# Performance work log

Hardware: AMD Instinct MI355X
Metric: run time of the kernel (lower is better)

Reference implementation:

```python
import jax, jax.numpy as jnp
import numpy as np

EPS = 1e-5

def conv2d(x, w, b=None, pad=1):
    y = jax.lax.conv_general_dilated(x, w, (1, 1), ((pad, pad), (pad, pad)),
                                     dimension_numbers=('NCHW', 'OIHW', 'NCHW'))
    if b is not None:
        y = y + b[None, :, None, None]
    return y

def batchnorm(x, g, b):
    # torch training-mode BN: per-channel batch mean / biased variance
    m = x.mean((0, 2, 3), keepdims=True)
    v = ((x - m) ** 2).mean((0, 2, 3), keepdims=True)
    return (x - m) * jax.lax.rsqrt(v + EPS) * g[None, :, None, None] + b[None, :, None, None]

def deform_conv(x, offset, w):
    # x: [B,C,H,W]; offset: [B,2*K*K,H,W] as (dy,dx) pairs per kernel tap; w: [O,C,K,K]
    B, C, H, W = x.shape
    O = w.shape[0]
    K = w.shape[-1]
    off = offset.reshape(B, K * K, 2, H, W)
    ki = jnp.arange(K)
    ky, kx = jnp.meshgrid(ki, ki, indexing='ij')
    ky = ky.reshape(-1).astype(x.dtype)  # [K*K]
    kx = kx.reshape(-1).astype(x.dtype)
    gy = jnp.arange(H, dtype=x.dtype)[None, None, :, None]
    gx = jnp.arange(W, dtype=x.dtype)[None, None, None, :]
    pad = (K - 1) // 2  # stride=1, pad=1, dilation=1
    py = gy + (ky - pad)[None, :, None, None] + off[:, :, 0]  # [B,K*K,H,W]
    px = gx + (kx - pad)[None, :, None, None] + off[:, :, 1]
    y0 = jnp.floor(py)
    x0 = jnp.floor(px)
    wy = py - y0
    wx = px - x0
    y0i = y0.astype(jnp.int32)
    x0i = x0.astype(jnp.int32)
    xf = x.reshape(B, C, H * W)

    def corner(yc, xc):
        valid = ((yc >= 0) & (yc < H) & (xc >= 0) & (xc < W)).astype(x.dtype)
        idx = jnp.clip(yc, 0, H - 1) * W + jnp.clip(xc, 0, W - 1)  # [B,K*K,H,W]
        g = jax.vmap(lambda im, ix: im[:, ix])(xf, idx)  # [B,C,K*K,H,W]
        return g * valid[:, None]

    v00 = corner(y0i, x0i)
    v01 = corner(y0i, x0i + 1)
    v10 = corner(y0i + 1, x0i)
    v11 = corner(y0i + 1, x0i + 1)
    wy_ = wy[:, None]
    wx_ = wx[:, None]
    samp = (v00 * (1 - wy_) * (1 - wx_) + v01 * (1 - wy_) * wx_
            + v10 * wy_ * (1 - wx_) + v11 * wy_ * wx_)  # [B,C,K*K,H,W]
    return jnp.einsum('bckhw,ock->bohw', samp, w.reshape(O, C, K * K))


def setup_inputs() -> dict:
    key = jax.random.key(0)
    ks = jax.random.split(key, 20)
    B, inC, H, W = 64, 3, 64, 64
    G = 1  # num_deformable_groups

    def u(k, shape, fan):
        s = 1.0 / np.sqrt(fan)
        return jax.random.uniform(k, shape, jnp.float32, -s, s)

    return {
        'x':   jax.random.normal(ks[0], (B, inC, H, W), jnp.float32),
        'w1':  u(ks[1], (8, inC, 3, 3), inC * 9),
        'g1':  jnp.ones((8,), jnp.float32),  'b1': jnp.zeros((8,), jnp.float32),
        'w2':  u(ks[2], (20, 8, 3, 3), 8 * 9), 'bc2': u(ks[3], (20,), 8 * 9),
        'g2':  jnp.ones((20,), jnp.float32), 'b2': jnp.zeros((20,), jnp.float32),
        'w3':  u(ks[4], (G * 18, 20, 3, 3), 20 * 9),
        'wd1': u(ks[5], (40, 20, 3, 3), 20 * 9),
        'g3':  jnp.ones((40,), jnp.float32), 'b3': jnp.zeros((40,), jnp.float32),
        'w4':  u(ks[6], (G * 18, 40, 3, 3), 40 * 9), 'bc4': u(ks[7], (G * 18,), 40 * 9),
        'wd2': u(ks[8], (64, 40, 3, 3), 40 * 9),
        'g4':  jnp.ones((64,), jnp.float32), 'b4': jnp.zeros((64,), jnp.float32),
        'fw':  u(ks[9], (10, 256), 256), 'fb': u(ks[10], (10,), 256),
    }


def reference(x, w1, g1, b1, w2, bc2, g2, b2, w3, wd1, g3, b3, w4, bc4, wd2, g4, b4, fw, fb):
    h = batchnorm(jax.nn.relu(conv2d(x, w1)), g1, b1)
    h = batchnorm(jax.nn.relu(conv2d(h, w2, bc2)), g2, b2)
    off1 = conv2d(h, w3)
    h = batchnorm(jax.nn.relu(deform_conv(h, off1, wd1)), g3, b3)
    off2 = conv2d(h, w4, bc4)
    h = batchnorm(jax.nn.relu(deform_conv(h, off2, wd2)), g4, b4)
    em = h
    B, C, H, W = h.shape
    # avg_pool2d kernel [H//2, W//2] (stride defaults to kernel) -> 2x2 output
    p = h.reshape(B, C, 2, H // 2, 2, W // 2).mean(axis=(3, 5))  # [B,C,2,2]
    logits = p.reshape(B, -1) @ fw.T + fb  # [B,10]
    return jax.nn.softmax(logits, axis=-1), em
```

## Files before the change

kernel.cpp:

```cpp
#include <hip/hip_runtime.h>

#define IMW 64
#define HW 4096
#define BATCH 64
#define NPIX (BATCH * HW)
#define TPB 512
#define PIXBLK 8

__device__ inline float bfbits(unsigned int hi16) {
    union { unsigned int i; float f; } v; v.i = hi16; return v.f;
}
__device__ inline float bf_lo(unsigned int u) { return bfbits(u << 16); }
__device__ inline float bf_hi(unsigned int u) { return bfbits(u & 0xffff0000u); }
__device__ inline unsigned short f2bf(float f) {
    union { float f; unsigned int i; } v; v.f = f;
    unsigned int i = v.i;
    i += 0x7fff + ((i >> 16) & 1);
    return (unsigned short)(i >> 16);
}

__device__ inline unsigned pack_h2(float a, float b) {
    union { unsigned u; _Float16 h[2]; } v;
    v.h[0] = (_Float16)a;
    v.h[1] = (_Float16)b;
    return v.u;
}
__device__ inline float h_lo(unsigned u) {
    union { unsigned u; _Float16 h[2]; } v; v.u = u; return (float)v.h[0];
}
__device__ inline float h_hi(unsigned u) {
    union { unsigned u; _Float16 h[2]; } v; v.u = u; return (float)v.h[1];
}

template <int CO_BLOCKS>
__device__ inline void swz(int lin, int& img, int& xblk, int& cob) {
    const int per_img = PIXBLK * CO_BLOCKS;
    int xcd = lin & 7;
    int s = lin >> 3;
    img = xcd * 8 + s / per_img;
    int r = s % per_img;
    cob = r / PIXBLK;
    xblk = r % PIXBLK;
}

template <int CIN, int COUT, bool RELU, bool BIAS, bool AFF, bool IN_NCHW,
          bool IN_BF16, int OUT_MODE>
__global__ void conv3x3_k(const void* __restrict__ in_,
                          const float* __restrict__ w,
                          const float* __restrict__ bias,
                          const float* __restrict__ iscale,
                          const float* __restrict__ ishift,
                          void* __restrict__ out_) {
    __shared__ float lw[9 * CIN * COUT];
    __shared__ float lb[COUT];
    __shared__ float lsc[CIN];
    __shared__ float lsh[CIN];

    for (int dst = threadIdx.x; dst < 9 * CIN * COUT; dst += blockDim.x) {
        int co = dst % COUT;
        int kci = dst / COUT;
        int k = kci / CIN;
        int ci = kci % CIN;
        lw[dst] = w[(size_t)co * (CIN * 9) + ci * 9 + k];
    }
    if (threadIdx.x < COUT) lb[threadIdx.x] = BIAS ? bias[threadIdx.x] : 0.f;
    if (AFF && threadIdx.x < CIN) {
        lsc[threadIdx.x] = iscale[threadIdx.x];
        lsh[threadIdx.x] = ishift[threadIdx.x];
    }
    __syncthreads();

    int img, xblk, cob;
    swz<1>(blockIdx.x, img, xblk, cob);
    int b = img;
    int pos = xblk * TPB + threadIdx.x;
    int p = (b << 12) + pos;
    int y = pos >> 6;
    int x = pos & 63;

    float acc[COUT];
#pragma unroll
    for (int co = 0; co < COUT; ++co) acc[co] = lb[co];

#pragma unroll 1
    for (int k = 0; k < 9; ++k) {
        int ky = k / 3, kx = k - ky * 3;
        int yy = y + ky - 1, xx = x + kx - 1;
        if (yy < 0 || yy >= IMW || xx < 0 || xx >= IMW) continue;

        float vin[CIN];
        if constexpr (IN_NCHW) {
            const float* ip = (const float*)in_;
#pragma unroll
            for (int ci = 0; ci < CIN; ++ci)
                vin[ci] = ip[((size_t)(b * CIN + ci) << 12) + yy * IMW + xx];
        } else if constexpr (!IN_BF16) {
            const float* ip = (const float*)in_ + ((size_t)((b << 12) + yy * IMW + xx)) * CIN;
#pragma unroll
            for (int c4 = 0; c4 < CIN / 4; ++c4) {
                float4 v = *(const float4*)(ip + c4 * 4);
                vin[c4 * 4 + 0] = v.x;
                vin[c4 * 4 + 1] = v.y;
                vin[c4 * 4 + 2] = v.z;
                vin[c4 * 4 + 3] = v.w;
            }
        } else if constexpr (CIN % 8 == 0) {
            const uint4* ip = (const uint4*)((const unsigned short*)in_ +
                                             ((size_t)((b << 12) + yy * IMW + xx)) * CIN);
#pragma unroll
            for (int c8 = 0; c8 < CIN / 8; ++c8) {
                uint4 u = ip[c8];
                vin[c8 * 8 + 0] = bf_lo(u.x); vin[c8 * 8 + 1] = bf_hi(u.x);
                vin[c8 * 8 + 2] = bf_lo(u.y); vin[c8 * 8 + 3] = bf_hi(u.y);
                vin[c8 * 8 + 4] = bf_lo(u.z); vin[c8 * 8 + 5] = bf_hi(u.z);
                vin[c8 * 8 + 6] = bf_lo(u.w); vin[c8 * 8 + 7] = bf_hi(u.w);
            }
        } else {
            const uint2* ip = (const uint2*)((const unsigned short*)in_ +
                                             ((size_t)((b << 12) + yy * IMW + xx)) * CIN);
#pragma unroll
            for (int c4 = 0; c4 < CIN / 4; ++c4) {
                uint2 u = ip[c4];
                vin[c4 * 4 + 0] = bf_lo(u.x); vin[c4 * 4 + 1] = bf_hi(u.x);
                vin[c4 * 4 + 2] = bf_lo(u.y); vin[c4 * 4 + 3] = bf_hi(u.y);
            }
        }
        if constexpr (AFF) {
#pragma unroll
            for (int ci = 0; ci < CIN; ++ci)
                vin[ci] = fmaf(vin[ci], lsc[ci], lsh[ci]);
        }
#pragma unroll
        for (int ci = 0; ci < CIN; ++ci) {
            float s = vin[ci];
            const float* wr = &lw[(k * CIN + ci) * COUT];
#pragma unroll
            for (int co = 0; co < COUT; ++co)
                acc[co] = fmaf(wr[co], s, acc[co]);
        }
    }

    if (RELU) {
#pragma unroll
        for (int co = 0; co < COUT; ++co) acc[co] = fmaxf(acc[co], 0.f);
    }

    if constexpr (OUT_MODE == 2) {
        unsigned* o = (unsigned*)out_;
#pragma unroll
        for (int i = 0; i < COUT / 2; ++i)
            o[(size_t)i * NPIX + p] = pack_h2(acc[2 * i], acc[2 * i + 1]);
    } else if constexpr (OUT_MODE == 1) {
        unsigned int us[COUT / 2];
#pragma unroll
        for (int i = 0; i < COUT / 2; ++i)
            us[i] = (unsigned int)f2bf(acc[2 * i]) | ((unsigned int)f2bf(acc[2 * i + 1]) << 16);
        uint2* o2 = (uint2*)((unsigned short*)out_ + (size_t)p * COUT);
#pragma unroll
        for (int i = 0; i < COUT / 4; ++i)
            o2[i] = make_uint2(us[2 * i], us[2 * i + 1]);
    } else {
        float* op = (float*)out_ + (size_t)p * COUT;
        if constexpr (COUT % 4 == 0) {
#pragma unroll
            for (int c4 = 0; c4 < COUT / 4; ++c4)
                *(float4*)(op + c4 * 4) =
                    make_float4(acc[c4 * 4], acc[c4 * 4 + 1], acc[c4 * 4 + 2], acc[c4 * 4 + 3]);
        } else {
#pragma unroll
            for (int c2 = 0; c2 < COUT / 2; ++c2)
                *(float2*)(op + c2 * 2) = make_float2(acc[c2 * 2], acc[c2 * 2 + 1]);
        }
    }
}

template <int CIN, int COUT_TOT, int COUT_BLK, int CO_BLOCKS, bool OUT_NCHW, bool PERTAP>
__global__ void deform_k(const void* __restrict__ in_,
                         const unsigned* __restrict__ off,
                         const float* __restrict__ w,
                         const float* __restrict__ iscale,
                         const float* __restrict__ ishift,
                         void* __restrict__ out_) {
    constexpr int WSLICE = CIN * COUT_BLK;
    constexpr int LWSZ = PERTAP ? 2 * WSLICE : 9 * WSLICE;
    __shared__ float lw[LWSZ];
    __shared__ float lsc[CIN];
    __shared__ float lsh[CIN];

    int img, xblk, cob;
    swz<CO_BLOCKS>(blockIdx.x, img, xblk, cob);
    int co_base = cob * COUT_BLK;

    if (threadIdx.x < CIN) {
        lsc[threadIdx.x] = iscale[threadIdx.x];
        lsh[threadIdx.x] = ishift[threadIdx.x];
    }

    const float* wsrc = nullptr;
    if constexpr (PERTAP) {
        wsrc = w + (size_t)(co_base + (threadIdx.x & (COUT_BLK - 1))) * (CIN * 9) +
               (threadIdx.x / COUT_BLK) * 9;
    } else {
        for (int dst = threadIdx.x; dst < 9 * WSLICE; dst += blockDim.x) {
            int co = dst % COUT_BLK;
            int kci = dst / COUT_BLK;
            int k = kci / CIN;
            int ci = kci % CIN;
            lw[dst] = w[(size_t)(co_base + co) * (CIN * 9) + ci * 9 + k];
        }
    }

    constexpr int NFULL = WSLICE / TPB;
    constexpr int REM = WSLICE - NFULL * TPB;
    constexpr int CISTEP = TPB / COUT_BLK;

    auto stage_tap = [&](int k, int buf) {
        if constexpr (PERTAP) {
            const float* src = wsrc + k;
            float* d = lw + buf * WSLICE + threadIdx.x;
#pragma unroll
            for (int j = 0; j < NFULL; ++j)
                d[j * TPB] = src[(size_t)j * CISTEP * 9];
            if (REM > 0 && threadIdx.x < REM)
                d[NFULL * TPB] = src[(size_t)NFULL * CISTEP * 9];
        }
    };

    if constexpr (PERTAP) stage_tap(0, 0);
    __syncthreads();

    int b = img;
    int pos = xblk * TPB + threadIdx.x;
    int p = (b << 12) + pos;
    int y = pos >> 6;
    int x = pos & 63;

    float acc[COUT_BLK];
#pragma unroll
    for (int co = 0; co < COUT_BLK; ++co) acc[co] = 0.f;

    unsigned od[9];
#pragma unroll
    for (int j = 0; j < 9; ++j) od[j] = off[(size_t)j * NPIX + p];

    const unsigned short* ib = (const unsigned short*)in_ + (size_t)b * HW * CIN;

#pragma unroll 1
    for (int k = 0; k < 9; ++k) {
        if constexpr (PERTAP) {
            if (k < 8) stage_tap(k + 1, (k + 1) & 1);
        }
        const int kbase = PERTAP ? (k & 1) * CIN : k * CIN;

        int ky = k / 3, kx = k - ky * 3;
        float py = (float)(y + ky - 1) + h_lo(od[k]);
        float px = (float)(x + kx - 1) + h_hi(od[k]);
        float fy = floorf(py), fx = floorf(px);
        float wy = py - fy, wx = px - fx;
        int y0 = (int)fy, x0 = (int)fx;
        int y1 = y0 + 1, x1 = x0 + 1;
        bool vy0 = (unsigned)y0 < (unsigned)IMW;
        bool vy1 = (unsigned)y1 < (unsigned)IMW;
        bool vx0 = (unsigned)x0 < (unsigned)IMW;
        bool vx1 = (unsigned)x1 < (unsigned)IMW;
        int cy0 = min(max(y0, 0), IMW - 1), cy1 = min(max(y1, 0), IMW - 1);
        int cx0 = min(max(x0, 0), IMW - 1), cx1 = min(max(x1, 0), IMW - 1);
        float w00 = (1.f - wy) * (1.f - wx) * ((vy0 & vx0) ? 1.f : 0.f);
        float w01 = (1.f - wy) * wx * ((vy0 & vx1) ? 1.f : 0.f);
        float w10 = wy * (1.f - wx) * ((vy1 & vx0) ? 1.f : 0.f);
        float w11 = wy * wx * ((vy1 & vx1) ? 1.f : 0.f);
        float wsum = w00 + w01 + w10 + w11;

        if constexpr (CIN % 8 == 0) {
            const uint4* q00 = (const uint4*)(ib + (size_t)(cy0 * IMW + cx0) * CIN);
            const uint4* q01 = (const uint4*)(ib + (size_t)(cy0 * IMW + cx1) * CIN);
            const uint4* q10 = (const uint4*)(ib + (size_t)(cy1 * IMW + cx0) * CIN);
            const uint4* q11 = (const uint4*)(ib + (size_t)(cy1 * IMW + cx1) * CIN);
#pragma unroll 1
            for (int c8 = 0; c8 < CIN / 8; ++c8) {
                uint4 a = q00[c8], bq = q01[c8], c = q10[c8], d = q11[c8];
#pragma unroll
                for (int h = 0; h < 4; ++h) {
                    unsigned int ua = (&a.x)[h], ub = (&bq.x)[h];
                    unsigned int uc = (&c.x)[h], ud = (&d.x)[h];
                    int ci0 = c8 * 8 + h * 2;
                    float r0 = w00 * bf_lo(ua) + w01 * bf_lo(ub) +
                               w10 * bf_lo(uc) + w11 * bf_lo(ud);
                    float r1 = w00 * bf_hi(ua) + w01 * bf_hi(ub) +
                               w10 * bf_hi(uc) + w11 * bf_hi(ud);
                    float s0 = fmaf(r0, lsc[ci0], lsh[ci0] * wsum);
                    float s1 = fmaf(r1, lsc[ci0 + 1], lsh[ci0 + 1] * wsum);
                    const float* wr0 = &lw[(kbase + ci0) * COUT_BLK];
                    const float* wr1 = &lw[(kbase + ci0 + 1) * COUT_BLK];
#pragma unroll
                    for (int co = 0; co < COUT_BLK; ++co)
                        acc[co] = fmaf(wr0[co], s0, acc[co]);
#pragma unroll
                    for (int co = 0; co < COUT_BLK; ++co)
                        acc[co] = fmaf(wr1[co], s1, acc[co]);
                }
            }
        } else {
            const uint2* q00 = (const uint2*)(ib + (size_t)(cy0 * IMW + cx0) * CIN);
            const uint2* q01 = (const uint2*)(ib + (size_t)(cy0 * IMW + cx1) * CIN);
            const uint2* q10 = (const uint2*)(ib + (size_t)(cy1 * IMW + cx0) * CIN);
            const uint2* q11 = (const uint2*)(ib + (size_t)(cy1 * IMW + cx1) * CIN);
#pragma unroll
            for (int c4 = 0; c4 < CIN / 4; ++c4) {
                uint2 a = q00[c4], bq = q01[c4], c = q10[c4], d = q11[c4];
#pragma unroll
                for (int h = 0; h < 2; ++h) {
                    unsigned int ua = (&a.x)[h], ub = (&bq.x)[h];
                    unsigned int uc = (&c.x)[h], ud = (&d.x)[h];
                    int ci0 = c4 * 4 + h * 2;
                    float r0 = w00 * bf_lo(ua) + w01 * bf_lo(ub) +
                               w10 * bf_lo(uc) + w11 * bf_lo(ud);
                    float r1 = w00 * bf_hi(ua) + w01 * bf_hi(ub) +
                               w10 * bf_hi(uc) + w11 * bf_hi(ud);
                    float s0 = fmaf(r0, lsc[ci0], lsh[ci0] * wsum);
                    float s1 = fmaf(r1, lsc[ci0 + 1], lsh[ci0 + 1] * wsum);
                    const float* wr0 = &lw[(kbase + ci0) * COUT_BLK];
                    const float* wr1 = &lw[(kbase + ci0 + 1) * COUT_BLK];
#pragma unroll
                    for (int co = 0; co < COUT_BLK; ++co)
                        acc[co] = fmaf(wr0[co], s0, acc[co]);
#pragma unroll
                    for (int co = 0; co < COUT_BLK; ++co)
                        acc[co] = fmaf(wr1[co], s1, acc[co]);
                }
            }
        }

        if constexpr (PERTAP) __syncthreads();
    }

#pragma unroll
    for (int co = 0; co < COUT_BLK; ++co) acc[co] = fmaxf(acc[co], 0.f);

    if constexpr (OUT_NCHW) {
        float* o = (float*)out_;
#pragma unroll
        for (int co = 0; co < COUT_BLK; ++co)
            __builtin_nontemporal_store(acc[co],
                &o[((size_t)(b * COUT_TOT + co_base + co) << 12) + pos]);
    } else {
        unsigned int us[COUT_BLK / 2];
#pragma unroll
        for (int i = 0; i < COUT_BLK / 2; ++i)
            us[i] = (unsigned int)f2bf(acc[2 * i]) | ((unsigned int)f2bf(acc[2 * i + 1]) << 16);
        unsigned short* ob = (unsigned short*)out_ + (size_t)p * COUT_TOT + co_base;
        if constexpr (COUT_BLK % 8 == 0) {
            uint4* o4 = (uint4*)ob;
#pragma unroll
            for (int i = 0; i < COUT_BLK / 8; ++i)
                o4[i] = make_uint4(us[4 * i], us[4 * i + 1], us[4 * i + 2], us[4 * i + 3]);
        } else {
            uint2* o2 = (uint2*)ob;
#pragma unroll
            for (int i = 0; i < COUT_BLK / 4; ++i)
                o2[i] = make_uint2(us[2 * i], us[2 * i + 1]);
        }
    }
}

template <int C>
__global__ void bn_partial_nhwc(const float* __restrict__ src, float* __restrict__ sums) {
    const size_t total = (size_t)NPIX * C;
    size_t stride = (size_t)gridDim.x * blockDim.x;
    float s = 0.f, q = 0.f;
    for (size_t i = (size_t)blockIdx.x * blockDim.x + threadIdx.x; i < total; i += stride) {
        float v = src[i];
        s += v;
        q += v * v;
    }
    __shared__ float ls[320], lq[320];
    ls[threadIdx.x] = s;
    lq[threadIdx.x] = q;
    __syncthreads();
    if (threadIdx.x < C) {
        float a = 0.f, bb = 0.f;
        for (int j = threadIdx.x; j < 320; j += C) {
            a += ls[j];
            bb += lq[j];
        }
        atomicAdd(&sums[threadIdx.x], a);
        atomicAdd(&sums[C + threadIdx.x], bb);
    }
}

template <int C>
__global__ void bn_partial_nhwc_bf16(const unsigned short* __restrict__ src,
                                     float* __restrict__ sums) {
    const int CP = C / 2;
    const size_t totalu = (size_t)NPIX * CP;
    const unsigned int* s32 = (const unsigned int*)src;
    size_t stride = (size_t)gridDim.x * blockDim.x;
    float s0 = 0.f, q0 = 0.f, s1 = 0.f, q1 = 0.f;
    for (size_t i = (size_t)blockIdx.x * blockDim.x + threadIdx.x; i < totalu; i += stride) {
        unsigned int u = s32[i];
        float a = bf_lo(u), b = bf_hi(u);
        s0 += a; q0 += a * a;
        s1 += b; q1 += b * b;
    }
    __shared__ float l0[320], m0[320], l1[320], m1[320];
    l0[threadIdx.x] = s0; m0[threadIdx.x] = q0;
    l1[threadIdx.x] = s1; m1[threadIdx.x] = q1;
    __syncthreads();
    if (threadIdx.x < C) {
        int cp = threadIdx.x >> 1, hi = threadIdx.x & 1;
        float a = 0.f, bb = 0.f;
        for (int j = cp; j < 320; j += CP) {
            a += hi ? l1[j] : l0[j];
            bb += hi ? m1[j] : m0[j];
        }
        atomicAdd(&sums[threadIdx.x], a);
        atomicAdd(&sums[C + threadIdx.x], bb);
    }
}

__global__ void bn_partial_nchw(const float* __restrict__ src, int C, int parts,
                                float* __restrict__ sums) {
    int c = blockIdx.x / parts;
    int part = blockIdx.x % parts;
    int chunk = NPIX / parts;
    int start = part * chunk;
    float s = 0.f, q = 0.f;
    for (int i4 = start / 4 + threadIdx.x; i4 < (start + chunk) / 4; i4 += blockDim.x) {
        int p4 = i4 * 4;
        int bb = p4 >> 12, pos = p4 & 4095;
        float4 v = *(const float4*)&src[((size_t)(bb * C + c) << 12) + pos];
        s += v.x + v.y + v.z + v.w;
        q += v.x * v.x + v.y * v.y + v.z * v.z + v.w * v.w;
    }
    __shared__ float ls[256], lq[256];
    ls[threadIdx.x] = s;
    lq[threadIdx.x] = q;
    __syncthreads();
    for (int st = 128; st > 0; st >>= 1) {
        if (threadIdx.x < st) {
            ls[threadIdx.x] += ls[threadIdx.x + st];
            lq[threadIdx.x] += lq[threadIdx.x + st];
        }
        __syncthreads();
    }
    if (threadIdx.x == 0) {
        atomicAdd(&sums[c], ls[0]);
        atomicAdd(&sums[C + c], lq[0]);
    }
}

__global__ void bn_finalize_kernel(const float* __restrict__ sums, int C,
                                   const float* __restrict__ g,
                                   const float* __restrict__ b,
                                   float* __restrict__ scale,
                                   float* __restrict__ shift) {
    int c = threadIdx.x;
    if (c >= C) return;
    const float invN = 1.f / (float)NPIX;
    float mean = sums[c] * invN;
    float var = sums[C + c] * invN - mean * mean;
    float sc = g[c] * rsqrtf(var + 1e-5f);
    scale[c] = sc;
    shift[c] = b[c] - mean * sc;
}

__global__ void bn4_apply_pool(float* __restrict__ em,
                               const float* __restrict__ scale,
                               const float* __restrict__ shift,
                               float* __restrict__ pw) {
    int bc = blockIdx.x;
    int c = bc & 63;
    int t = threadIdx.x;
    float sc = scale[c], sh = shift[c];
    float* base = em + ((size_t)bc << 12);
    int pos = t * 16;
    int quad = ((pos >= 2048) ? 2 : 0) + ((pos & 63) >> 5);
    float s = 0.f;
#pragma unroll
    for (int k4 = 0; k4 < 4; ++k4) {
        float4 v = *(float4*)(base + pos + k4 * 4);
        v.x = fmaf(v.x, sc, sh);
        v.y = fmaf(v.y, sc, sh);
        v.z = fmaf(v.z, sc, sh);
        v.w = fmaf(v.w, sc, sh);
        *(float4*)(base + pos + k4 * 4) = v;
        s += v.x + v.y + v.z + v.w;
    }
    __shared__ float qs[4];
    if (t < 4) qs[t] = 0.f;
    __syncthreads();
    atomicAdd(&qs[quad], s);
    __syncthreads();
    if (t < 4) pw[bc * 4 + t] = qs[t] * (1.f / 1024.f);
}

__global__ void fc_softmax_kernel(const float* __restrict__ pw,
                                  const float* __restrict__ fw,
                                  const float* __restrict__ fb,
                                  float* __restrict__ out) {
    int b = blockIdx.x;
    int t = threadIdx.x;
    __shared__ float logits[10];
    if (t < 10) {
        float acc = fb[t];
        const float* p = pw + b * 256;
        for (int q = 0; q < 256; ++q) acc = fmaf(p[q], fw[t * 256 + q], acc);
        logits[t] = acc;
    }
    __syncthreads();
    if (t == 0) {
        float m = -1e30f;
        for (int q = 0; q < 10; ++q) m = fmaxf(m, logits[q]);
        float e[10], sum = 0.f;
        for (int q = 0; q < 10; ++q) { e[q] = expf(logits[q] - m); sum += e[q]; }
        float inv = 1.f / sum;
        for (int q = 0; q < 10; ++q) out[b * 10 + q] = e[q] * inv;
    }
}

extern "C" void kernel_launch(void* const* d_in, const int* in_sizes, int n_in,
                              void* d_out, int out_size, void* d_ws, size_t ws_size,
                              hipStream_t stream) {
    (void)in_sizes; (void)n_in; (void)out_size; (void)ws_size;

    const float* x   = (const float*)d_in[0];
    const float* w1  = (const float*)d_in[1];
    const float* g1  = (const float*)d_in[2];
    const float* b1  = (const float*)d_in[3];
    const float* w2  = (const float*)d_in[4];
    const float* bc2 = (const float*)d_in[5];
    const float* g2  = (const float*)d_in[6];
    const float* b2  = (const float*)d_in[7];
    const float* w3  = (const float*)d_in[8];
    const float* wd1 = (const float*)d_in[9];
    const float* g3  = (const float*)d_in[10];
    const float* b3  = (const float*)d_in[11];
    const float* w4  = (const float*)d_in[12];
    const float* bc4 = (const float*)d_in[13];
    const float* wd2 = (const float*)d_in[14];
    const float* g4  = (const float*)d_in[15];
    const float* b4  = (const float*)d_in[16];
    const float* fw  = (const float*)d_in[17];
    const float* fb  = (const float*)d_in[18];

    float* out = (float*)d_out;
    float* softout = out;
    float* em = out + 640;

    float* ws = (float*)d_ws;
    float* h1 = ws;
    unsigned short* h2b = (unsigned short*)(h1 + (size_t)2097152);
    unsigned short* h3b = h2b + (size_t)5242880;
    unsigned* offu = (unsigned*)(h3b + (size_t)10485760);
    float* sums1 = (float*)(offu + (size_t)9 * NPIX);
    float* sums2 = sums1 + 128;
    float* sums3 = sums2 + 128;
    float* sums4 = sums3 + 128;
    float* scale = sums4 + 128;
    float* shift = scale + 64;
    float* pw = shift + 64;

    dim3 blk(TPB);
    dim3 gpix(BATCH * PIXBLK);

    hipMemsetAsync(sums1, 0, 4 * 128 * sizeof(float), stream);

    conv3x3_k<3, 8, true, false, false, true, false, 0>
        <<<gpix, blk, 0, stream>>>(x, w1, nullptr, nullptr, nullptr, h1);
    bn_partial_nhwc<8><<<256, 320, 0, stream>>>(h1, sums1);
    bn_finalize_kernel<<<1, 64, 0, stream>>>(sums1, 8, g1, b1, scale, shift);

    conv3x3_k<8, 20, true, true, true, false, false, 1>
        <<<gpix, blk, 0, stream>>>(h1, w2, bc2, scale, shift, h2b);
    bn_partial_nhwc_bf16<20><<<256, 320, 0, stream>>>(h2b, sums2);
    bn_finalize_kernel<<<1, 64, 0, stream>>>(sums2, 20, g2, b2, scale, shift);

    conv3x3_k<20, 18, false, false, true, false, true, 2>
        <<<gpix, blk, 0, stream>>>(h2b, w3, nullptr, scale, shift, offu);
    deform_k<20, 40, 20, 2, false, false>
        <<<dim3(BATCH * PIXBLK * 2), blk, 0, stream>>>(h2b, offu, wd1, scale, shift, h3b);
    bn_partial_nhwc_bf16<40><<<256, 320, 0, stream>>>(h3b, sums3);
    bn_finalize_kernel<<<1, 64, 0, stream>>>(sums3, 40, g3, b3, scale, shift);

    conv3x3_k<40, 18, false, true, true, false, true, 2>
        <<<gpix, blk, 0, stream>>>(h3b, w4, bc4, scale, shift, offu);
    deform_k<40, 64, 32, 2, true, true>
        <<<dim3(BATCH * PIXBLK * 2), blk, 0, stream>>>(h3b, offu, wd2, scale, shift, em);
    bn_partial_nchw<<<64 * 32, 256, 0, stream>>>(em, 64, 32, sums4);
    bn_finalize_kernel<<<1, 64, 0, stream>>>(sums4, 64, g4, b4, scale, shift);

    bn4_apply_pool<<<64 * 64, 256, 0, stream>>>(em, scale, shift, pw);
    fc_softmax_kernel<<<64, 64, 0, stream>>>(pw, fw, fb, softout);
}
```

Before: 594.2 us.

## Fuse BN statistics into conv/deform epilogues and stage final output in fp16

Removes the separate BN partial-sum kernels. Each conv and deform kernel now computes per-channel sum and sum-of-squares with wave shuffles and shared-memory atomics, then adds them into global sums with atomics. The last deform conv writes an fp16 raw buffer, which the apply/pool kernel reads and expands to fp32 em. This avoids re-reading the large intermediates but adds fp16 rounding to the final activations and many global atomics.

```diff
diff --git a/kernel.cpp b/kernel.cpp
--- a/kernel.cpp
+++ b/kernel.cpp
@@ -30,6 +30,9 @@
 }
 __device__ inline float h_hi(unsigned u) {
     union { unsigned u; _Float16 h[2]; } v; v.u = u; return (float)v.h[1];
+}
+__device__ inline unsigned short f2h(float f) {
+    union { _Float16 h; unsigned short u; } v; v.h = (_Float16)f; return v.u;
 }
 
 template <int CO_BLOCKS>
@@ -44,17 +47,19 @@
 }
 
 template <int CIN, int COUT, bool RELU, bool BIAS, bool AFF, bool IN_NCHW,
-          bool IN_BF16, int OUT_MODE>
+          bool IN_BF16, int OUT_MODE, bool FUSE_BN>
 __global__ void conv3x3_k(const void* __restrict__ in_,
                           const float* __restrict__ w,
                           const float* __restrict__ bias,
                           const float* __restrict__ iscale,
                           const float* __restrict__ ishift,
-                          void* __restrict__ out_) {
+                          void* __restrict__ out_,
+                          float* __restrict__ bnsums) {
     __shared__ float lw[9 * CIN * COUT];
     __shared__ float lb[COUT];
     __shared__ float lsc[CIN];
     __shared__ float lsh[CIN];
+    __shared__ float bnacc[FUSE_BN ? 2 * COUT : 1];
 
     for (int dst = threadIdx.x; dst < 9 * CIN * COUT; dst += blockDim.x) {
         int co = dst % COUT;
@@ -68,6 +73,7 @@
         lsc[threadIdx.x] = iscale[threadIdx.x];
         lsh[threadIdx.x] = ishift[threadIdx.x];
     }
+    if (FUSE_BN && threadIdx.x < 2 * COUT) bnacc[threadIdx.x] = 0.f;
     __syncthreads();
 
     int img, xblk, cob;
@@ -145,6 +151,23 @@
         for (int co = 0; co < COUT; ++co) acc[co] = fmaxf(acc[co], 0.f);
     }
 
+    if constexpr (FUSE_BN) {
+#pragma unroll
+        for (int co = 0; co < COUT; ++co) {
+            float s = acc[co];
+            float q = s * s;
+#pragma unroll
+            for (int off = 32; off; off >>= 1) {
+                s += __shfl_down(s, off, 64);
+                q += __shfl_down(q, off, 64);
+            }
+            if ((threadIdx.x & 63) == 0) {
+                atomicAdd(&bnacc[co], s);
+                atomicAdd(&bnacc[COUT + co], q);
+            }
+        }
+    }
+
     if constexpr (OUT_MODE == 2) {
         unsigned* o = (unsigned*)out_;
 #pragma unroll
@@ -172,20 +195,31 @@
                 *(float2*)(op + c2 * 2) = make_float2(acc[c2 * 2], acc[c2 * 2 + 1]);
         }
     }
-}
-
-template <int CIN, int COUT_TOT, int COUT_BLK, int CO_BLOCKS, bool OUT_NCHW, bool PERTAP>
+
+    if constexpr (FUSE_BN) {
+        __syncthreads();
+        if (threadIdx.x < COUT)
+            atomicAdd(&bnsums[threadIdx.x], bnacc[threadIdx.x]);
+        else if (threadIdx.x < 2 * COUT)
+            atomicAdd(&bnsums[threadIdx.x], bnacc[threadIdx.x]);
+    }
+}
+
+template <int CIN, int COUT_TOT, int COUT_BLK, int CO_BLOCKS, bool OUT_NCHW,
+          bool PERTAP, bool FUSE>
 __global__ void deform_k(const void* __restrict__ in_,
                          const unsigned* __restrict__ off,
                          const float* __restrict__ w,
                          const float* __restrict__ iscale,
                          const float* __restrict__ ishift,
-                         void* __restrict__ out_) {
+                         void* __restrict__ out_,
+                         float* __restrict__ bnsums) {
     constexpr int WSLICE = CIN * COUT_BLK;
     constexpr int LWSZ = PERTAP ? 2 * WSLICE : 9 * WSLICE;
     __shared__ float lw[LWSZ];
     __shared__ float lsc[CIN];
     __shared__ float lsh[CIN];
+    __shared__ float bnacc[FUSE ? 2 * COUT_BLK : 1];
 
     int img, xblk, cob;
     swz<CO_BLOCKS>(blockIdx.x, img, xblk, cob);
@@ -195,6 +229,7 @@
         lsc[threadIdx.x] = iscale[threadIdx.x];
         lsh[threadIdx.x] = ishift[threadIdx.x];
     }
+    if (FUSE && threadIdx.x < 2 * COUT_BLK) bnacc[threadIdx.x] = 0.f;
 
     const float* wsrc = nullptr;
     if constexpr (PERTAP) {
@@ -337,11 +372,28 @@
 #pragma unroll
     for (int co = 0; co < COUT_BLK; ++co) acc[co] = fmaxf(acc[co], 0.f);
 
+    if constexpr (FUSE) {
+#pragma unroll
+        for (int co = 0; co < COUT_BLK; ++co) {
+            float s = acc[co];
+            float q = s * s;
+#pragma unroll
+            for (int off2 = 32; off2; off2 >>= 1) {
+                s += __shfl_down(s, off2, 64);
+                q += __shfl_down(q, off2, 64);
+            }
+            if ((threadIdx.x & 63) == 0) {
+                atomicAdd(&bnacc[co], s);
+                atomicAdd(&bnacc[COUT_BLK + co], q);
+            }
+        }
+    }
+
     if constexpr (OUT_NCHW) {
-        float* o = (float*)out_;
+        unsigned short* o = (unsigned short*)out_;
 #pragma unroll
         for (int co = 0; co < COUT_BLK; ++co)
-            __builtin_nontemporal_store(acc[co],
+            __builtin_nontemporal_store(f2h(acc[co]),
                 &o[((size_t)(b * COUT_TOT + co_base + co) << 12) + pos]);
     } else {
         unsigned int us[COUT_BLK / 2];
@@ -361,91 +413,14 @@
                 o2[i] = make_uint2(us[2 * i], us[2 * i + 1]);
         }
     }
-}
-
-template <int C>
-__global__ void bn_partial_nhwc(const float* __restrict__ src, float* __restrict__ sums) {
-    const size_t total = (size_t)NPIX * C;
-    size_t stride = (size_t)gridDim.x * blockDim.x;
-    float s = 0.f, q = 0.f;
-    for (size_t i = (size_t)blockIdx.x * blockDim.x + threadIdx.x; i < total; i += stride) {
-        float v = src[i];
-        s += v;
-        q += v * v;
-    }
-    __shared__ float ls[320], lq[320];
-    ls[threadIdx.x] = s;
-    lq[threadIdx.x] = q;
-    __syncthreads();
-    if (threadIdx.x < C) {
-        float a = 0.f, bb = 0.f;
-        for (int j = threadIdx.x; j < 320; j += C) {
-            a += ls[j];
-            bb += lq[j];
-        }
-        atomicAdd(&sums[threadIdx.x], a);
-        atomicAdd(&sums[C + threadIdx.x], bb);
-    }
-}
-
-template <int C>
-__global__ void bn_partial_nhwc_bf16(const unsigned short* __restrict__ src,
-                                     float* __restrict__ sums) {
-    const int CP = C / 2;
-    const size_t totalu = (size_t)NPIX * CP;
-    const unsigned int* s32 = (const unsigned int*)src;
-    size_t stride = (size_t)gridDim.x * blockDim.x;
-    float s0 = 0.f, q0 = 0.f, s1 = 0.f, q1 = 0.f;
-    for (size_t i = (size_t)blockIdx.x * blockDim.x + threadIdx.x; i < totalu; i += stride) {
-        unsigned int u = s32[i];
-        float a = bf_lo(u), b = bf_hi(u);
-        s0 += a; q0 += a * a;
-        s1 += b; q1 += b * b;
-    }
-    __shared__ float l0[320], m0[320], l1[320], m1[320];
-    l0[threadIdx.x] = s0; m0[threadIdx.x] = q0;
-    l1[threadIdx.x] = s1; m1[threadIdx.x] = q1;
-    __syncthreads();
-    if (threadIdx.x < C) {
-        int cp = threadIdx.x >> 1, hi = threadIdx.x & 1;
-        float a = 0.f, bb = 0.f;
-        for (int j = cp; j < 320; j += CP) {
-            a += hi ? l1[j] : l0[j];
-            bb += hi ? m1[j] : m0[j];
-        }
-        atomicAdd(&sums[threadIdx.x], a);
-        atomicAdd(&sums[C + threadIdx.x], bb);
-    }
-}
-
-__global__ void bn_partial_nchw(const float* __restrict__ src, int C, int parts,
-                                float* __restrict__ sums) {
-    int c = blockIdx.x / parts;
-    int part = blockIdx.x % parts;
-    int chunk = NPIX / parts;
-    int start = part * chunk;
-    float s = 0.f, q = 0.f;
-    for (int i4 = start / 4 + threadIdx.x; i4 < (start + chunk) / 4; i4 += blockDim.x) {
-        int p4 = i4 * 4;
-        int bb = p4 >> 12, pos = p4 & 4095;
-        float4 v = *(const float4*)&src[((size_t)(bb * C + c) << 12) + pos];
-        s += v.x + v.y + v.z + v.w;
-        q += v.x * v.x + v.y * v.y + v.z * v.z + v.w * v.w;
-    }
-    __shared__ float ls[256], lq[256];
-    ls[threadIdx.x] = s;
-    lq[threadIdx.x] = q;
-    __syncthreads();
-    for (int st = 128; st > 0; st >>= 1) {
-        if (threadIdx.x < st) {
-            ls[threadIdx.x] += ls[threadIdx.x + st];
-            lq[threadIdx.x] += lq[threadIdx.x + st];
-        }
+
+    if constexpr (FUSE) {
         __syncthreads();
-    }
-    if (threadIdx.x == 0) {
-        atomicAdd(&sums[c], ls[0]);
-        atomicAdd(&sums[C + c], lq[0]);
+        if (threadIdx.x < COUT_BLK)
+            atomicAdd(&bnsums[co_base + threadIdx.x], bnacc[threadIdx.x]);
+        else if (threadIdx.x < 2 * COUT_BLK)
+            atomicAdd(&bnsums[COUT_TOT + co_base + (threadIdx.x - COUT_BLK)],
+                      bnacc[threadIdx.x]);
     }
 }
 
@@ -464,27 +439,30 @@
     shift[c] = b[c] - mean * sc;
 }
 
-__global__ void bn4_apply_pool(float* __restrict__ em,
+__global__ void bn4_apply_pool(const unsigned short* __restrict__ raw,
                                const float* __restrict__ scale,
                                const float* __restrict__ shift,
+                               float* __restrict__ em,
                                float* __restrict__ pw) {
     int bc = blockIdx.x;
     int c = bc & 63;
     int t = threadIdx.x;
     float sc = scale[c], sh = shift[c];
+    const unsigned* rb = (const unsigned*)(raw + ((size_t)bc << 12));
     float* base = em + ((size_t)bc << 12);
     int pos = t * 16;
     int quad = ((pos >= 2048) ? 2 : 0) + ((pos & 63) >> 5);
     float s = 0.f;
 #pragma unroll
-    for (int k4 = 0; k4 < 4; ++k4) {
-        float4 v = *(float4*)(base + pos + k4 * 4);
-        v.x = fmaf(v.x, sc, sh);
-        v.y = fmaf(v.y, sc, sh);
-        v.z = fmaf(v.z, sc, sh);
-        v.w = fmaf(v.w, sc, sh);
-        *(float4*)(base + pos + k4 * 4) = v;
-        s += v.x + v.y + v.z + v.w;
+    for (int g = 0; g < 2; ++g) {
+        uint4 u = *(const uint4*)(rb + (pos >> 1) + g * 4);
+        float f0 = fmaf(h_lo(u.x), sc, sh), f1 = fmaf(h_hi(u.x), sc, sh);
+        float f2 = fmaf(h_lo(u.y), sc, sh), f3 = fmaf(h_hi(u.y), sc, sh);
+        float f4 = fmaf(h_lo(u.z), sc, sh), f5 = fmaf(h_hi(u.z), sc, sh);
+        float f6 = fmaf(h_lo(u.w), sc, sh), f7 = fmaf(h_hi(u.w), sc, sh);
+        *(float4*)(base + pos + g * 8) = make_float4(f0, f1, f2, f3);
+        *(float4*)(base + pos + g * 8 + 4) = make_float4(f4, f5, f6, f7);
+        s += f0 + f1 + f2 + f3 + f4 + f5 + f6 + f7;
     }
     __shared__ float qs[4];
     if (t < 4) qs[t] = 0.f;
@@ -552,7 +530,8 @@
     unsigned short* h2b = (unsigned short*)(h1 + (size_t)2097152);
     unsigned short* h3b = h2b + (size_t)5242880;
     unsigned* offu = (unsigned*)(h3b + (size_t)10485760);
-    float* sums1 = (float*)(offu + (size_t)9 * NPIX);
+    unsigned short* emraw = (unsigned short*)(offu + (size_t)9 * NPIX);
+    float* sums1 = (float*)(emraw + (size_t)16777216);
     float* sums2 = sums1 + 128;
     float* sums3 = sums2 + 128;
     float* sums4 = sums3 + 128;
@@ -565,30 +544,26 @@
 
     hipMemsetAsync(sums1, 0, 4 * 128 * sizeof(float), stream);
 
-    conv3x3_k<3, 8, true, false, false, true, false, 0>
-        <<<gpix, blk, 0, stream>>>(x, w1, nullptr, nullptr, nullptr, h1);
-    bn_partial_nhwc<8><<<256, 320, 0, stream>>>(h1, sums1);
+    conv3x3_k<3, 8, true, false, false, true, false, 0, true>
+        <<<gpix, blk, 0, stream>>>(x, w1, nullptr, nullptr, nullptr, h1, sums1);
     bn_finalize_kernel<<<1, 64, 0, stream>>>(sums1, 8, g1, b1, scale, shift);
 
-    conv3x3_k<8, 20, true, true, true, false, false, 1>
-        <<<gpix, blk, 0, stream>>>(h1, w2, bc2, scale, shift, h2b);
-    bn_partial_nhwc_bf16<20><<<256, 320, 0, stream>>>(h2b, sums2);
+    conv3x3_k<8, 20, true, true, true, false, false, 1, true>
+        <<<gpix, blk, 0, stream>>>(h1, w2, bc2, scale, shift, h2b, sums2);
     bn_finalize_kernel<<<1, 64, 0, stream>>>(sums2, 20, g2, b2, scale, shift);
 
-    conv3x3_k<20, 18, false, false, true, false, true, 2>
-        <<<gpix, blk, 0, stream>>>(h2b, w3, nullptr, scale, shift, offu);
-    deform_k<20, 40, 20, 2, false, false>
-        <<<dim3(BATCH * PIXBLK * 2), blk, 0, stream>>>(h2b, offu, wd1, scale, shift, h3b);
-    bn_partial_nhwc_bf16<40><<<256, 320, 0, stream>>>(h3b, sums3);
+    conv3x3_k<20, 18, false, false, true, false, true, 2, false>
+        <<<gpix, blk, 0, stream>>>(h2b, w3, nullptr, scale, shift, offu, nullptr);
+    deform_k<20, 40, 20, 2, false, false, true>
+        <<<dim3(BATCH * PIXBLK * 2), blk, 0, stream>>>(h2b, offu, wd1, scale, shift, h3b, sums3);
     bn_finalize_kernel<<<1, 64, 0, stream>>>(sums3, 40, g3, b3, scale, shift);
 
-    conv3x3_k<40, 18, false, true, true, false, true, 2>
-        <<<gpix, blk, 0, stream>>>(h3b, w4, bc4, scale, shift, offu);
-    deform_k<40, 64, 32, 2, true, true>
-        <<<dim3(BATCH * PIXBLK * 2), blk, 0, stream>>>(h3b, offu, wd2, scale, shift, em);
-    bn_partial_nchw<<<64 * 32, 256, 0, stream>>>(em, 64, 32, sums4);
+    conv3x3_k<40, 18, false, true, true, false, true, 2, false>
+        <<<gpix, blk, 0, stream>>>(h3b, w4, bc4, scale, shift, offu, nullptr);
+    deform_k<40, 64, 32, 2, true, true, true>
+        <<<dim3(BATCH * PIXBLK * 2), blk, 0, stream>>>(h3b, offu, wd2, scale, shift, emraw, sums4);
     bn_finalize_kernel<<<1, 64, 0, stream>>>(sums4, 64, g4, b4, scale, shift);
 
-    bn4_apply_pool<<<64 * 64, 256, 0, stream>>>(em, scale, shift, pw);
+    bn4_apply_pool<<<64 * 64, 256, 0, stream>>>(emraw, scale, shift, em, pw);
     fc_softmax_kernel<<<64, 64, 0, stream>>>(pw, fw, fb, softout);
 }
```

Result: no change. 595.5 us (+0.2%).
